# Kernel optimization log

Hardware: AMD Instinct MI355X
Metric: run time of the kernel (lower is better)

Reference implementation:

```python
import jax, jax.numpy as jnp
import numpy as np

T, S, B, H, E, I = 64, 400, 32, 512, 1024, 128


def setup_inputs() -> dict:
    key = jax.random.key(0)
    ks = jax.random.split(key, 16)
    def n(k, shape, scale=1.0):
        return jax.random.normal(k, shape, dtype=jnp.float32) * scale
    return {
        "embedded_y": n(ks[0], (T, B, I)),
        "encode_outputs": n(ks[1], (S, B, E)),
        "init_state": n(ks[2], (B, H)),
        "x_mask": jnp.ones((S, B, 1), jnp.float32),
        "y_mask": jnp.ones((T, B, 1), jnp.float32),
        "x_index": jax.random.randint(ks[3], (S, B), 0, 50000, dtype=jnp.int32),
        "init_coverage": jnp.zeros((B, S), jnp.float32),
        # attention params
        "W_h": n(ks[4], (E, E), E ** -0.5),
        "W_s": n(ks[5], (E, H), H ** -0.5),
        "W_c": n(ks[6], (E, 1), 1.0),
        "b_attn": n(ks[7], (E,), 0.02),
        "V": n(ks[8], (1, E), E ** -0.5),
        # gru1: input I -> hidden H (torch gate order r, z, n)
        "w_ih1": n(ks[9], (3 * H, I), I ** -0.5),
        "w_hh1": n(ks[10], (3 * H, H), H ** -0.5),
        "b_ih1": jnp.zeros((3 * H,), jnp.float32),
        "b_hh1": jnp.zeros((3 * H,), jnp.float32),
        # gru2: input E(=2H) -> hidden H
        "w_ih2": n(ks[11], (3 * H, E), E ** -0.5),
        "w_hh2": n(ks[12], (3 * H, H), H ** -0.5),
        "b_ih2": jnp.zeros((3 * H,), jnp.float32),
        "b_hh2": jnp.zeros((3 * H,), jnp.float32),
    }


def _gru_cell(x, h, w_ih, w_hh, b_ih, b_hh):
    # single-step nn.GRU (torch gate order: r, z, n)
    gi = x @ w_ih.T + b_ih
    gh = h @ w_hh.T + b_hh
    i_r, i_z, i_n = jnp.split(gi, 3, axis=-1)
    h_r, h_z, h_n = jnp.split(gh, 3, axis=-1)
    r = jax.nn.sigmoid(i_r + h_r)
    z = jax.nn.sigmoid(i_z + h_z)
    n_ = jnp.tanh(i_n + r * h_n)
    return (1.0 - z) * n_ + z * h


def reference(embedded_y, encode_outputs, init_state, x_mask, y_mask, x_index,
              init_coverage, W_h, W_s, W_c, b_attn, V,
              w_ih1, w_hh1, b_ih1, b_hh1, w_ih2, w_hh2, b_ih2, b_hh2):
    # hoist the encoder projection out of the time loop (loop-invariant)
    Wh_enc = jnp.einsum('sbe,fe->sbf', encode_outputs, W_h)  # [S,B,E]
    wc = W_c[:, 0]  # [E], since W_c: Linear(1, E)

    def step(carry, inp):
        hidden, cov = carry          # [B,H], [B,S]
        y_t, ym = inp                # [B,I], [B,1]
        s1 = _gru_cell(y_t, hidden, w_ih1, w_hh1, b_ih1, b_hh1)
        s1 = ym * s1 + (1.0 - ym) * hidden
        # Bahdanau attention with coverage
        states = Wh_enc + (s1 @ W_s.T)[None, :, :] + cov.T[:, :, None] * wc + b_attn  # [S,B,E]
        score = (jnp.tanh(states) * x_mask) @ V.T            # [S,B,1]
        score = jnp.where(x_mask == 0, -1e9, score)
        aw = jax.nn.softmax(score, axis=0)                   # softmax over source positions
        ctx = jnp.sum(aw * encode_outputs, axis=0)           # [B,E]
        s2 = _gru_cell(ctx, s1, w_ih2, w_hh2, b_ih2, b_hh2)
        s2 = ym * s2 + (1.0 - ym) * s1
        wa = aw[:, :, 0].T                                   # [B,S]
        return (s2, cov + wa), (s2, ctx, wa, cov)

    _, (hidden_states, context_vectors, words_attention_weights, coverage_vectors) = \
        jax.lax.scan(step, (init_state, init_coverage), (embedded_y, y_mask))
    Tn = embedded_y.shape[0]
    x_index_t = x_index.T  # [B,S]
    x_indexes = jnp.broadcast_to(x_index_t[None], (Tn,) + x_index_t.shape)
    # is_predicting=False: coverage BEFORE each step (coverage_vectors_all[:-1])
    return (hidden_states, context_vectors, words_attention_weights, x_indexes, coverage_vectors)
```

## Files before the change

### kernel.cpp

```cpp
#include <hip/hip_runtime.h>
#include <cstdint>
#include <cstddef>

#define T_ 64
#define S_ 400
#define B_ 32
#define H_ 512
#define E_ 1024
#define I_ 128

__device__ __forceinline__ float sigmoid_(float x){ return 1.0f/(1.0f + __expf(-x)); }
__device__ __forceinline__ float tanh_(float x){
    float e = __expf(2.0f*fabsf(x));
    float t = 1.0f - 2.0f/(e + 1.0f);
    return copysignf(t, x);
}


__global__ __launch_bounds__(256) void init_kernel(const float* __restrict__ init_state,
        const float* __restrict__ init_cov, float* __restrict__ h0, float* __restrict__ cov){
    int i = blockIdx.x*256 + threadIdx.x;
    if (i < B_*H_) h0[i] = init_state[i];
    if (i < B_*S_) cov[i] = init_cov[i];
}

__global__ __launch_bounds__(256) void xidx_kernel(const int* __restrict__ x_index, float* __restrict__ out){
    int i = blockIdx.x*256 + threadIdx.x;
    if (i >= T_*B_*S_) return;
    int s = i % S_;
    int b = (i / S_) % B_;
    out[i] = (float)x_index[s*B_ + b];
}

#define BM 64
#define BN 64
#define BK 16
__global__ __launch_bounds__(256) void gemm_whenc(const float* __restrict__ A,
        const float* __restrict__ Bw, float* __restrict__ C){
    __shared__ float As[BK][BM];
    __shared__ float Bs[BK][BN];
    int bm = blockIdx.x;
    int bn = blockIdx.y;
    int tid = threadIdx.x;
    int lrow  = tid >> 2;
    int lcol4 = (tid & 3) * 4;
    int tx = tid & 15, ty = tid >> 4;
    const float* Ab = A  + (size_t)(bm*BM)*1024;
    const float* Bb = Bw + (size_t)(bn*BN)*1024;
    float acc[4][4] = {};
    for (int k0 = 0; k0 < 1024; k0 += BK){
        float4 av = *(const float4*)(Ab + (size_t)lrow*1024 + k0 + lcol4);
        float4 bv = *(const float4*)(Bb + (size_t)lrow*1024 + k0 + lcol4);
        As[lcol4+0][lrow]=av.x; As[lcol4+1][lrow]=av.y; As[lcol4+2][lrow]=av.z; As[lcol4+3][lrow]=av.w;
        Bs[lcol4+0][lrow]=bv.x; Bs[lcol4+1][lrow]=bv.y; Bs[lcol4+2][lrow]=bv.z; Bs[lcol4+3][lrow]=bv.w;
        __syncthreads();
        #pragma unroll
        for (int kk = 0; kk < BK; ++kk){
            float4 a4 = *(const float4*)&As[kk][ty*4];
            float4 b4 = *(const float4*)&Bs[kk][tx*4];
            float a_[4] = {a4.x, a4.y, a4.z, a4.w};
            float b_[4] = {b4.x, b4.y, b4.z, b4.w};
            #pragma unroll
            for (int i=0;i<4;++i)
                #pragma unroll
                for (int j=0;j<4;++j) acc[i][j] = fmaf(a_[i], b_[j], acc[i][j]);
        }
        __syncthreads();
    }
    int m0 = bm*BM + ty*4, n0 = bn*BN + tx*4;
    #pragma unroll
    for (int i=0;i<4;++i){
        float4 o = make_float4(acc[i][0], acc[i][1], acc[i][2], acc[i][3]);
        *(float4*)&C[(size_t)(m0+i)*E_ + n0] = o;
    }
}


__global__ __launch_bounds__(256) void gru1_kernel(const float* __restrict__ y,
        const float* __restrict__ hid,
        const float* __restrict__ w_ih, const float* __restrict__ w_hh,
        const float* __restrict__ b_ih, const float* __restrict__ b_hh,
        const float* __restrict__ ymask, float* __restrict__ s1, int t){
    __shared__ float xs[I_];
    __shared__ float hs[H_];
    __shared__ float part[3][64][6];
    int tid = threadIdx.x;
    int b = blockIdx.y;
    int hh = tid & 63, p = tid >> 6;
    int h = blockIdx.x*64 + hh;
    for (int i=tid; i<I_; i+=256) xs[i] = y[(size_t)t*B_*I_ + (size_t)b*I_ + i];
    for (int i=tid; i<H_; i+=256) hs[i] = hid[(size_t)b*H_ + i];
    __syncthreads();
    float gp[6];
    #pragma unroll
    for (int g=0; g<3; ++g){
        const float* wr = w_ih + (size_t)(g*H_ + h)*I_;
        float acc = 0.0f;
        for (int k = p*32; k < p*32 + 32; k += 4){
            float4 w4 = *(const float4*)(wr + k);
            acc = fmaf(w4.x, xs[k+0], acc); acc = fmaf(w4.y, xs[k+1], acc);
            acc = fmaf(w4.z, xs[k+2], acc); acc = fmaf(w4.w, xs[k+3], acc);
        }
        gp[g] = acc;
    }
    #pragma unroll
    for (int g=0; g<3; ++g){
        const float* wr = w_hh + (size_t)(g*H_ + h)*H_;
        float acc = 0.0f;
        for (int k = p*128; k < p*128 + 128; k += 4){
            float4 w4 = *(const float4*)(wr + k);
            acc = fmaf(w4.x, hs[k+0], acc); acc = fmaf(w4.y, hs[k+1], acc);
            acc = fmaf(w4.z, hs[k+2], acc); acc = fmaf(w4.w, hs[k+3], acc);
        }
        gp[3+g] = acc;
    }
    if (p){ 
        #pragma unroll
        for (int j=0;j<6;++j) part[p-1][hh][j] = gp[j]; 
    }
    __syncthreads();
    if (p == 0){
        float gi[3], gh[3];
        #pragma unroll
        for (int j=0;j<3;++j) gi[j] = gp[j]   + part[0][hh][j]   + part[1][hh][j]   + part[2][hh][j]   + b_ih[j*H_ + h];
        #pragma unroll
        for (int j=0;j<3;++j) gh[j] = gp[3+j] + part[0][hh][3+j] + part[1][hh][3+j] + part[2][hh][3+j] + b_hh[j*H_ + h];
        float r = sigmoid_(gi[0] + gh[0]);
        float z = sigmoid_(gi[1] + gh[1]);
        float n = tanh_(gi[2] + r*gh[2]);
        float hv = hs[h];
        float sv = (1.0f - z)*n + z*hv;
        float ym = ymask[t*B_ + b];
        s1[(size_t)b*H_ + h] = ym*sv + (1.0f - ym)*hv;
    }
}

__global__ __launch_bounds__(256) void qproj_kernel(const float* __restrict__ s1,
        const float* __restrict__ W_s, const float* __restrict__ b_attn, float* __restrict__ qb){
    __shared__ float hs[H_];
    __shared__ float part[3][64];
    int tid = threadIdx.x;
    int b = blockIdx.y;
    int ff = tid & 63, p = tid >> 6;
    int f = blockIdx.x*64 + ff;
    for (int i=tid; i<H_; i+=256) hs[i] = s1[(size_t)b*H_ + i];
    __syncthreads();
    const float* wr = W_s + (size_t)f*H_;
    float acc = 0.0f;
    for (int k = p*128; k < p*128 + 128; k += 4){
        float4 w4 = *(const float4*)(wr + k);
        acc = fmaf(w4.x, hs[k+0], acc); acc = fmaf(w4.y, hs[k+1], acc);
        acc = fmaf(w4.z, hs[k+2], acc); acc = fmaf(w4.w, hs[k+3], acc);
    }
    if (p) part[p-1][ff] = acc;
    __syncthreads();
    if (p == 0) qb[(size_t)b*E_ + f] = acc + part[0][ff] + part[1][ff] + part[2][ff] + b_attn[f];
}

__global__ __launch_bounds__(256) void score_kernel(const float* __restrict__ whenc,
        const float* __restrict__ qb, const float* __restrict__ cov,
        const float* __restrict__ wc, const float* __restrict__ Vv,
        const float* __restrict__ xmask, float* __restrict__ scores){
    int wave = blockIdx.x*4 + (threadIdx.x >> 6);
    int lane = threadIdx.x & 63;
    int s = wave >> 5, b = wave & 31;
    const float* wp = whenc + (size_t)(s*B_ + b)*E_;
    const float* qp = qb + (size_t)b*E_;
    float cv = cov[b*S_ + s];
    float acc = 0.0f;
    #pragma unroll
    for (int i=0;i<4;++i){
        int e = (i*64 + lane)*4;
        float4 w4 = *(const float4*)(wp + e);
        float4 q4 = *(const float4*)(qp + e);
        float4 c4 = *(const float4*)(wc + e);
        float4 v4 = *(const float4*)(Vv + e);
        acc = fmaf(v4.x, tanh_(w4.x + q4.x + cv*c4.x), acc);
        acc = fmaf(v4.y, tanh_(w4.y + q4.y + cv*c4.y), acc);
        acc = fmaf(v4.z, tanh_(w4.z + q4.z + cv*c4.z), acc);
        acc = fmaf(v4.w, tanh_(w4.w + q4.w + cv*c4.w), acc);
    }
    #pragma unroll
    for (int off=32; off; off>>=1) acc += __shfl_xor(acc, off);
    if (lane == 0){
        float xm = xmask[s*B_ + b];
        scores[s*B_ + b] = (xm == 0.0f) ? -1e9f : acc*xm;
    }
}

__global__ __launch_bounds__(128) void attn_ctx_kernel(const float* __restrict__ scores,
        const float* __restrict__ enc, float* __restrict__ cov, float* __restrict__ ctxbuf,
        float* __restrict__ out_ctx, float* __restrict__ out_wa, float* __restrict__ out_cov, int t){
    __shared__ float p[S_];
    __shared__ float red[4];
    int tid = threadIdx.x;
    int b = blockIdx.x >> 3;
    int chunk = blockIdx.x & 7;
    float v[4];
    #pragma unroll
    for (int i=0;i<4;++i){
        int s = tid + i*128;
        v[i] = (s < S_) ? scores[s*B_ + b] : -1e30f;
    }
    float mx = fmaxf(fmaxf(v[0],v[1]), fmaxf(v[2],v[3]));
    #pragma unroll
    for (int off=32; off; off>>=1) mx = fmaxf(mx, __shfl_xor(mx, off));
    if ((tid & 63) == 0) red[tid >> 6] = mx;
    __syncthreads();
    mx = fmaxf(red[0], red[1]);
    float ev[4];
    float sm = 0.0f;
    #pragma unroll
    for (int i=0;i<4;++i){
        int s = tid + i*128;
        ev[i] = (s < S_) ? __expf(v[i] - mx) : 0.0f;
        sm += ev[i];
    }
    #pragma unroll
    for (int off=32; off; off>>=1) sm += __shfl_xor(sm, off);
    if ((tid & 63) == 0) red[2 + (tid >> 6)] = sm;
    __syncthreads();
    float rden = 1.0f/(red[2] + red[3]);
    #pragma unroll
    for (int i=0;i<4;++i){
        int s = tid + i*128;
        if (s < S_) p[s] = ev[i]*rden;
    }
    __syncthreads();
    int e = chunk*128 + tid;
    const float* ep = enc + (size_t)b*E_ + e;
    float acc = 0.0f;
    #pragma unroll 4
    for (int s=0; s<S_; ++s) acc = fmaf(p[s], ep[(size_t)s*(B_*E_)], acc);
    ctxbuf[(size_t)b*E_ + e] = acc;
    out_ctx[(size_t)t*B_*E_ + (size_t)b*E_ + e] = acc;
    if (chunk == 0){
        for (int s=tid; s<S_; s+=128){
            float c = cov[b*S_ + s];
            out_wa [(size_t)t*B_*S_ + (size_t)b*S_ + s] = p[s];
            out_cov[(size_t)t*B_*S_ + (size_t)b*S_ + s] = c;
            cov[b*S_ + s] = c + p[s];
        }
    }
}

__global__ __launch_bounds__(256) void gru2_kernel(const float* __restrict__ ctx,
        const float* __restrict__ s1,
        const float* __restrict__ w_ih, const float* __restrict__ w_hh,
        const float* __restrict__ b_ih, const float* __restrict__ b_hh,
        const float* __restrict__ ymask, float* __restrict__ hnext,
        float* __restrict__ out_hidden, int t){
    __shared__ float xs[E_];
    __shared__ float hs[H_];
    __shared__ float part[3][64][6];
    int tid = threadIdx.x;
    int b = blockIdx.y;
    int hh = tid & 63, p = tid >> 6;
    int h = blockIdx.x*64 + hh;
    for (int i=tid; i<E_; i+=256) xs[i] = ctx[(size_t)b*E_ + i];
    for (int i=tid; i<H_; i+=256) hs[i] = s1[(size_t)b*H_ + i];
    __syncthreads();
    float gp[6];
    #pragma unroll
    for (int g=0; g<3; ++g){
        const float* wr = w_ih + (size_t)(g*H_ + h)*E_;
        float acc = 0.0f;
        for (int k = p*256; k < p*256 + 256; k += 4){
            float4 w4 = *(const float4*)(wr + k);
            acc = fmaf(w4.x, xs[k+0], acc); acc = fmaf(w4.y, xs[k+1], acc);
            acc = fmaf(w4.z, xs[k+2], acc); acc = fmaf(w4.w, xs[k+3], acc);
        }
        gp[g] = acc;
    }
    #pragma unroll
    for (int g=0; g<3; ++g){
        const float* wr = w_hh + (size_t)(g*H_ + h)*H_;
        float acc = 0.0f;
        for (int k = p*128; k < p*128 + 128; k += 4){
            float4 w4 = *(const float4*)(wr + k);
            acc = fmaf(w4.x, hs[k+0], acc); acc = fmaf(w4.y, hs[k+1], acc);
            acc = fmaf(w4.z, hs[k+2], acc); acc = fmaf(w4.w, hs[k+3], acc);
        }
        gp[3+g] = acc;
    }
    if (p){ 
        #pragma unroll
        for (int j=0;j<6;++j) part[p-1][hh][j] = gp[j]; 
    }
    __syncthreads();
    if (p == 0){
        float gi[3], gh[3];
        #pragma unroll
        for (int j=0;j<3;++j) gi[j] = gp[j]   + part[0][hh][j]   + part[1][hh][j]   + part[2][hh][j]   + b_ih[j*H_ + h];
        #pragma unroll
        for (int j=0;j<3;++j) gh[j] = gp[3+j] + part[0][hh][3+j] + part[1][hh][3+j] + part[2][hh][3+j] + b_hh[j*H_ + h];
        float r = sigmoid_(gi[0] + gh[0]);
        float z = sigmoid_(gi[1] + gh[1]);
        float n = tanh_(gi[2] + r*gh[2]);
        float s1v = hs[h];
        float sv = (1.0f - z)*n + z*s1v;
        float ym = ymask[t*B_ + b];
        float o = ym*sv + (1.0f - ym)*s1v;
        hnext[(size_t)b*H_ + h] = o;
        out_hidden[(size_t)t*B_*H_ + (size_t)b*H_ + h] = o;
    }
}


extern "C" void kernel_launch(void* const* d_in, const int* in_sizes, int n_in,
                              void* d_out, int out_size, void* d_ws, size_t ws_size,
                              hipStream_t stream) {
    const float* y          = (const float*)d_in[0];
    const float* enc        = (const float*)d_in[1];
    const float* init_state = (const float*)d_in[2];
    const float* xmask      = (const float*)d_in[3];
    const float* ymask      = (const float*)d_in[4];
    const int*   x_index    = (const int*)  d_in[5];
    const float* init_cov   = (const float*)d_in[6];
    const float* W_h        = (const float*)d_in[7];
    const float* W_s        = (const float*)d_in[8];
    const float* W_c        = (const float*)d_in[9];
    const float* b_attn     = (const float*)d_in[10];
    const float* Vv         = (const float*)d_in[11];
    const float* w_ih1      = (const float*)d_in[12];
    const float* w_hh1      = (const float*)d_in[13];
    const float* b_ih1      = (const float*)d_in[14];
    const float* b_hh1      = (const float*)d_in[15];
    const float* w_ih2      = (const float*)d_in[16];
    const float* w_hh2      = (const float*)d_in[17];
    const float* b_ih2      = (const float*)d_in[18];
    const float* b_hh2      = (const float*)d_in[19];

    float* out        = (float*)d_out;
    float* out_hidden = out;
    float* out_ctx    = out_hidden + (size_t)T_*B_*H_;
    float* out_wa     = out_ctx    + (size_t)T_*B_*E_;
    float* out_xidx   = out_wa     + (size_t)T_*B_*S_;
    float* out_cov    = out_xidx   + (size_t)T_*B_*S_;

    float* ws     = (float*)d_ws;
    float* whenc  = ws;
    float* qb     = whenc  + (size_t)S_*B_*E_;
    float* s1     = qb     + (size_t)B_*E_;
    float* h0     = s1     + (size_t)B_*H_;
    float* h1     = h0     + (size_t)B_*H_;
    float* cov    = h1     + (size_t)B_*H_;
    float* scores = cov    + (size_t)B_*S_;
    float* ctxbuf = scores + (size_t)S_*B_;

    init_kernel<<<64, 256, 0, stream>>>(init_state, init_cov, h0, cov);
    xidx_kernel<<<3200, 256, 0, stream>>>(x_index, out_xidx);
    gemm_whenc<<<dim3(200, 16), 256, 0, stream>>>(enc, W_h, whenc);

    for (int t = 0; t < T_; ++t){
        float* hcur  = (t & 1) ? h1 : h0;
        float* hnext = (t & 1) ? h0 : h1;
        gru1_kernel<<<dim3(8, 32), 256, 0, stream>>>(y, hcur, w_ih1, w_hh1, b_ih1, b_hh1, ymask, s1, t);
        qproj_kernel<<<dim3(16, 32), 256, 0, stream>>>(s1, W_s, b_attn, qb);
        score_kernel<<<3200, 256, 0, stream>>>(whenc, qb, cov, W_c, Vv, xmask, scores);
        attn_ctx_kernel<<<256, 128, 0, stream>>>(scores, enc, cov, ctxbuf, out_ctx, out_wa, out_cov, t);
        gru2_kernel<<<dim3(8, 32), 256, 0, stream>>>(ctxbuf, s1, w_ih2, w_hh2, b_ih2, b_hh2, ymask, hnext, out_hidden, t);
    }
}
```

Baseline: 8.539 ms.

## Split attention context reduction over source chunks across waves with transposed scores

The score kernel now writes scores in [B,S] layout so the softmax reads them contiguously per batch. The context kernel switches from 256 blocks of 128 threads, each summing all 400 source positions for one output element, to 512 blocks of 256 threads. In each block, four waves each cover 100 source positions for 64 output elements and combine partial sums through shared memory. This shortens the serial dependent load chain and raises parallelism and memory-level concurrency, at the cost of each block redoing the softmax and an extra reduction step.

```diff
diff --git a/kernel.cpp b/kernel.cpp
--- a/kernel.cpp
+++ b/kernel.cpp
@@ -160,7 +160,7 @@
 __global__ __launch_bounds__(256) void score_kernel(const float* __restrict__ whenc,
         const float* __restrict__ qb, const float* __restrict__ cov,
         const float* __restrict__ wc, const float* __restrict__ Vv,
-        const float* __restrict__ xmask, float* __restrict__ scores){
+        const float* __restrict__ xmask, float* __restrict__ scores_t){
     int wave = blockIdx.x*4 + (threadIdx.x >> 6);
     int lane = threadIdx.x & 63;
     int s = wave >> 5, b = wave & 31;
@@ -184,58 +184,55 @@
     for (int off=32; off; off>>=1) acc += __shfl_xor(acc, off);
     if (lane == 0){
         float xm = xmask[s*B_ + b];
-        scores[s*B_ + b] = (xm == 0.0f) ? -1e9f : acc*xm;
-    }
-}
-
-__global__ __launch_bounds__(128) void attn_ctx_kernel(const float* __restrict__ scores,
+        scores_t[b*S_ + s] = (xm == 0.0f) ? -1e9f : acc*xm;
+    }
+}
+
+__global__ __launch_bounds__(256) void ctx_kernel(const float* __restrict__ scores_t,
         const float* __restrict__ enc, float* __restrict__ cov, float* __restrict__ ctxbuf,
         float* __restrict__ out_ctx, float* __restrict__ out_wa, float* __restrict__ out_cov, int t){
     __shared__ float p[S_];
-    __shared__ float red[4];
-    int tid = threadIdx.x;
-    int b = blockIdx.x >> 3;
-    int chunk = blockIdx.x & 7;
-    float v[4];
-    #pragma unroll
-    for (int i=0;i<4;++i){
-        int s = tid + i*128;
-        v[i] = (s < S_) ? scores[s*B_ + b] : -1e30f;
-    }
-    float mx = fmaxf(fmaxf(v[0],v[1]), fmaxf(v[2],v[3]));
+    __shared__ float sacc[4][64];
+    __shared__ float red[8];
+    int tid = threadIdx.x;
+    int b  = blockIdx.y;
+    int e0 = blockIdx.x * 64;
+    float v0 = scores_t[b*S_ + tid];
+    float v1 = (tid + 256 < S_) ? scores_t[b*S_ + tid + 256] : -1e30f;
+    float mx = fmaxf(v0, v1);
     #pragma unroll
     for (int off=32; off; off>>=1) mx = fmaxf(mx, __shfl_xor(mx, off));
-    if ((tid & 63) == 0) red[tid >> 6] = mx;
-    __syncthreads();
-    mx = fmaxf(red[0], red[1]);
-    float ev[4];
-    float sm = 0.0f;
-    #pragma unroll
-    for (int i=0;i<4;++i){
-        int s = tid + i*128;
-        ev[i] = (s < S_) ? __expf(v[i] - mx) : 0.0f;
-        sm += ev[i];
-    }
+    int wid = tid >> 6, lane = tid & 63;
+    if (lane == 0) red[wid] = mx;
+    __syncthreads();
+    mx = fmaxf(fmaxf(red[0], red[1]), fmaxf(red[2], red[3]));
+    float e0v = __expf(v0 - mx);
+    float e1v = (tid + 256 < S_) ? __expf(v1 - mx) : 0.0f;
+    float sm = e0v + e1v;
     #pragma unroll
     for (int off=32; off; off>>=1) sm += __shfl_xor(sm, off);
-    if ((tid & 63) == 0) red[2 + (tid >> 6)] = sm;
-    __syncthreads();
-    float rden = 1.0f/(red[2] + red[3]);
-    #pragma unroll
-    for (int i=0;i<4;++i){
-        int s = tid + i*128;
-        if (s < S_) p[s] = ev[i]*rden;
-    }
-    __syncthreads();
-    int e = chunk*128 + tid;
-    const float* ep = enc + (size_t)b*E_ + e;
+    if (lane == 0) red[4 + wid] = sm;
+    __syncthreads();
+    float rden = 1.0f/(red[4] + red[5] + red[6] + red[7]);
+    p[tid] = e0v * rden;
+    if (tid + 256 < S_) p[tid + 256] = e1v * rden;
+    __syncthreads();
+    const float* ep = enc + (size_t)b*E_ + e0 + lane;
     float acc = 0.0f;
+    int sbeg = wid*100, send = sbeg + 100;
     #pragma unroll 4
-    for (int s=0; s<S_; ++s) acc = fmaf(p[s], ep[(size_t)s*(B_*E_)], acc);
-    ctxbuf[(size_t)b*E_ + e] = acc;
-    out_ctx[(size_t)t*B_*E_ + (size_t)b*E_ + e] = acc;
-    if (chunk == 0){
-        for (int s=tid; s<S_; s+=128){
+    for (int s = sbeg; s < send; ++s)
+        acc = fmaf(p[s], ep[(size_t)s*(B_*E_)], acc);
+    sacc[wid][lane] = acc;
+    __syncthreads();
+    if (wid == 0){
+        float a = sacc[0][lane] + sacc[1][lane] + sacc[2][lane] + sacc[3][lane];
+        int e = e0 + lane;
+        ctxbuf[(size_t)b*E_ + e] = a;
+        out_ctx[(size_t)t*B_*E_ + (size_t)b*E_ + e] = a;
+    }
+    if (blockIdx.x == 0){
+        for (int s = tid; s < S_; s += 256){
             float c = cov[b*S_ + s];
             out_wa [(size_t)t*B_*S_ + (size_t)b*S_ + s] = p[s];
             out_cov[(size_t)t*B_*S_ + (size_t)b*S_ + s] = c;
@@ -346,7 +343,7 @@
     float* h1     = h0     + (size_t)B_*H_;
     float* cov    = h1     + (size_t)B_*H_;
     float* scores = cov    + (size_t)B_*S_;
-    float* ctxbuf = scores + (size_t)S_*B_;
+    float* ctxbuf = scores + (size_t)B_*S_;
 
     init_kernel<<<64, 256, 0, stream>>>(init_state, init_cov, h0, cov);
     xidx_kernel<<<3200, 256, 0, stream>>>(x_index, out_xidx);
@@ -358,7 +355,7 @@
         gru1_kernel<<<dim3(8, 32), 256, 0, stream>>>(y, hcur, w_ih1, w_hh1, b_ih1, b_hh1, ymask, s1, t);
         qproj_kernel<<<dim3(16, 32), 256, 0, stream>>>(s1, W_s, b_attn, qb);
         score_kernel<<<3200, 256, 0, stream>>>(whenc, qb, cov, W_c, Vv, xmask, scores);
-        attn_ctx_kernel<<<256, 128, 0, stream>>>(scores, enc, cov, ctxbuf, out_ctx, out_wa, out_cov, t);
+        ctx_kernel<<<dim3(16, 32), 256, 0, stream>>>(scores, enc, cov, ctxbuf, out_ctx, out_wa, out_cov, t);
         gru2_kernel<<<dim3(8, 32), 256, 0, stream>>>(ctxbuf, s1, w_ih2, w_hh2, b_ih2, b_hh2, ymask, hnext, out_hidden, t);
     }
 }
```

After: 7.281 ms. 1.17x faster.
